# Kernel optimization log

Measured on AMD Instinct MI355X. Metric: run time of the kernel, lower is better.

The kernel has to match this reference:

```python
import jax, jax.numpy as jnp
import numpy as np

B, F, H = 512, 64, 256
INPUT_LEN, TARGET_LEN = 128, 128


def _gru_step(h, xt, Wih, Whh, bih, bhh):
    # PyTorch GRU cell: gates ordered [r, z, n]
    gi = xt @ Wih.T + bih            # [B, 3H]
    gh = h @ Whh.T + bhh             # [B, 3H]
    ir, iz, inn = jnp.split(gi, 3, axis=-1)
    hr, hz, hn = jnp.split(gh, 3, axis=-1)
    r = jax.nn.sigmoid(ir + hr)
    z = jax.nn.sigmoid(iz + hz)
    n = jnp.tanh(inn + r * hn)
    return (1.0 - z) * n + z * h


def setup_inputs() -> dict:
    key = jax.random.key(0)
    ks = jax.random.split(key, 12)
    s_in = 1.0 / np.sqrt(H)
    x = jax.random.normal(ks[0], (B, INPUT_LEN + TARGET_LEN, F), dtype=jnp.float32)
    u = lambda k, shp: jax.random.uniform(k, shp, jnp.float32, -s_in, s_in)
    return {
        "x": x,
        "enc_Wih": u(ks[1], (3 * H, F)), "enc_Whh": u(ks[2], (3 * H, H)),
        "enc_bih": u(ks[3], (3 * H,)), "enc_bhh": u(ks[4], (3 * H,)),
        "dec_Wih": u(ks[5], (3 * H, F)), "dec_Whh": u(ks[6], (3 * H, H)),
        "dec_bih": u(ks[7], (3 * H,)), "dec_bhh": u(ks[8], (3 * H,)),
        "reg_W": u(ks[9], (F, H)), "reg_b": u(ks[10], (F,)),
        "input_len": INPUT_LEN, "target_len": TARGET_LEN,
    }


def reference(x, enc_Wih, enc_Whh, enc_bih, enc_bhh,
              dec_Wih, dec_Whh, dec_bih, dec_bhh,
              reg_W, reg_b, input_len, target_len):
    source_seq = x[:, :input_len, :]                       # [B, Tin, F]
    b = source_seq.shape[0]

    # Encoder GRU over source sequence, h0 = 0
    def enc_step(h, xt):
        h = _gru_step(h, xt, enc_Wih, enc_Whh, enc_bih, enc_bhh)
        return h, None
    h0 = jnp.zeros((b, enc_Whh.shape[1]), dtype=x.dtype)
    h_enc, _ = jax.lax.scan(enc_step, h0, source_seq.transpose(1, 0, 2))

    # Decoder: eval mode -> teacher forcing prob 0, always feed back own output
    dec_in0 = source_seq[:, -1, :]                         # [B, F]
    def dec_step(carry, _):
        h, inp = carry
        h = _gru_step(h, inp, dec_Wih, dec_Whh, dec_bih, dec_bhh)
        out = h @ reg_W.T + reg_b                          # [B, F]
        return (h, out), out
    (_, _), outs = jax.lax.scan(dec_step, (h_enc, dec_in0), None, length=target_len)
    return outs.transpose(1, 0, 2)                         # [B, Tout, F]
```

## Files before the change

### kernel.cpp

```cpp
#include <hip/hip_runtime.h>
#include <math.h>

#define Bsz 512
#define Fsz 64
#define Hsz 256
#define TSTEPS 128
#define G3 768

#define BG 16
#define HB 16
#define NBLK 256
#define NTHR 256
#define CNT_STRIDE 512
#define POLLER 192

#define AP 264
#define XAP 72

#define OFF_AH  0
#define OFF_AL  16896
#define OFF_XH  33792
#define OFF_XL  38400
#define OFF_RED 43008
#define OFF_B   75776
#define SMEM_BYTES (OFF_B + 512)

typedef float f32x4 __attribute__((ext_vector_type(4)));
typedef short s16x8 __attribute__((ext_vector_type(8)));
typedef unsigned short u16x4 __attribute__((ext_vector_type(4)));
typedef unsigned int  u32x4 __attribute__((ext_vector_type(4)));

#define MF(a,b,c) __builtin_amdgcn_mfma_f32_16x16x32_bf16(a,b,c,0,0,0)

static __device__ __forceinline__ unsigned short bf16_rne(float f){
    union { float f; unsigned u; } v; v.f = f;
    return (unsigned short)((v.u + 0x7FFFu + ((v.u >> 16) & 1u)) >> 16);
}
static __device__ __forceinline__ float bf16_to_f(unsigned short h){
    union { unsigned u; float f; } v; v.u = ((unsigned)h) << 16; return v.f;
}
static __device__ __forceinline__ void split8(const float* p, s16x8& hi, s16x8& lo){
    #pragma unroll
    for (int t = 0; t < 8; ++t){
        float f = p[t];
        unsigned short h = bf16_rne(f);
        hi[t] = (short)h;
        lo[t] = (short)bf16_rne(f - bf16_to_f(h));
    }
}
static __device__ __forceinline__ float sigmoidf_(float v){ return 1.0f/(1.0f + expf(-v)); }

__device__ __forceinline__ u32x4 load_sys_b128u(const unsigned* p){
    u32x4 r;
    asm volatile("global_load_dwordx4 %0, %1, off sc0 sc1" : "=v"(r) : "v"(p) : "memory");
    return r;
}
__device__ __forceinline__ void store_sys_b32u(unsigned* p, unsigned v){
    asm volatile("global_store_dword %0, %1, off sc0 sc1" :: "v"(p), "v"(v) : "memory");
}
__device__ __forceinline__ int load_sys_i32(const int* p){
    int r;
    asm volatile("global_load_dword %0, %1, off sc0 sc1\n\ts_waitcnt vmcnt(0)"
                 : "=v"(r) : "v"(p) : "memory");
    return r;
}
__device__ __forceinline__ void waitcnt0(){ asm volatile("s_waitcnt vmcnt(0)" ::: "memory"); }
__device__ __forceinline__ void regbar(u32x4& v){ asm volatile("" : "+v"(v)); }

extern "C" __global__ void gru_setup(const float* __restrict__ x,
                                     const float* __restrict__ dWih,
                                     const float* __restrict__ dbih,
                                     const float* __restrict__ regW,
                                     const float* __restrict__ regb,
                                     float* __restrict__ Mw,
                                     float* __restrict__ cfold,
                                     float* __restrict__ gi0)
{
    int idx = blockIdx.x*blockDim.x + threadIdx.x;
    if (idx < G3*Hsz) {
        int g = idx >> 8, j = idx & 255;
        float a = 0.f;
        #pragma unroll 8
        for (int f = 0; f < Fsz; ++f) a += dWih[g*Fsz + f]*regW[f*Hsz + j];
        Mw[idx] = a;
    } else if (idx < G3*Hsz + G3) {
        int g = idx - G3*Hsz;
        float a = dbih[g];
        #pragma unroll 8
        for (int f = 0; f < Fsz; ++f) a += dWih[g*Fsz + f]*regb[f];
        cfold[g] = a;
    } else {
        int e = idx - (G3*Hsz + G3);
        if (e < Bsz*G3) {
            int b = e / G3, g = e - b*G3;
            const float* xp = x + (size_t)b*(256*64) + 127*64;
            float a = dbih[g];
            #pragma unroll 8
            for (int f = 0; f < Fsz; ++f) a += xp[f]*dWih[g*Fsz + f];
            gi0[e] = a;
        }
    }
}

extern "C" __global__ void __launch_bounds__(NTHR, 1)
gru_persistent(const float* __restrict__ x,
               const float* __restrict__ eWih, const float* __restrict__ eWhh,
               const float* __restrict__ ebih, const float* __restrict__ ebhh,
               const float* __restrict__ dWhh, const float* __restrict__ dbhh,
               const float* __restrict__ Mw,   const float* __restrict__ cfold,
               const float* __restrict__ gi0,  const float* __restrict__ regW,
               const float* __restrict__ regb,
               unsigned* __restrict__ hbuf, int* __restrict__ cnt,
               float* __restrict__ out)
{
    extern __shared__ char lds[];
    unsigned short* s_ah = (unsigned short*)(lds + OFF_AH);
    unsigned short* s_al = (unsigned short*)(lds + OFF_AL);
    unsigned short* s_xh = (unsigned short*)(lds + OFF_XH);
    unsigned short* s_xl = (unsigned short*)(lds + OFF_XL);
    float* s_red  = (float*)(lds + OFF_RED);
    float* s_bias = (float*)(lds + OFF_B);
    float* s_dbh  = s_bias + 64;
    float* s_b3   = s_bias + 112;

    const int tid  = threadIdx.x;
    const int wv   = tid >> 6;
    const int lane = tid & 63;
    const int quad = lane >> 4;
    const int lcol = lane & 15;
    const int bg   = blockIdx.x >> 4;
    const int hb   = blockIdx.x & 15;
    const int hcol = hb*16 + lcol;
    int* mycnt = cnt + bg*CNT_STRIDE;
    const f32x4 z4 = {0.f, 0.f, 0.f, 0.f};

    s16x8 wfh[3][2], wfl[3][2];
    s16x8 ufh[3], ufl[3];
    #pragma unroll
    for (int g = 0; g < 3; ++g)
        #pragma unroll
        for (int q = 0; q < 2; ++q)
            split8(eWhh + (size_t)(g*256 + hcol)*256 + wv*64 + q*32 + quad*8,
                   wfh[g][q], wfl[g][q]);
    if (wv < 2){
        #pragma unroll
        for (int g = 0; g < 3; ++g)
            split8(eWih + (size_t)(g*256 + hcol)*64 + wv*32 + quad*8, ufh[g], ufl[g]);
    }
    if (tid < 16){
        int c = hb*16 + tid;
        s_bias[tid]    = ebih[c]       + ebhh[c];
        s_bias[16+tid] = ebih[256+c]   + ebhh[256+c];
        s_bias[32+tid] = ebih[512+c];
        s_bias[48+tid] = ebhh[512+c];
    }
    __syncthreads();

    int parity = 0;

    for (int s = 0; s < TSTEPS; ++s) {
        f32x4 aR[2], aZ[2], aNi[2], aNh[2];
        if (wv == 0){
            float bR = s_bias[lcol], bZ = s_bias[16+lcol];
            float bNi = s_bias[32+lcol], bNh = s_bias[48+lcol];
            #pragma unroll
            for (int m = 0; m < 2; ++m){
                aR[m] = (f32x4){bR,bR,bR,bR}; aZ[m] = (f32x4){bZ,bZ,bZ,bZ};
                aNi[m] = (f32x4){bNi,bNi,bNi,bNi}; aNh[m] = (f32x4){bNh,bNh,bNh,bNh};
            }
        } else {
            #pragma unroll
            for (int m = 0; m < 2; ++m){ aR[m]=z4; aZ[m]=z4; aNi[m]=z4; aNh[m]=z4; }
        }

        #pragma unroll
        for (int jj = 0; jj < 2; ++jj){
            int flat = (wv*2 + jj)*64 + lane;
            int row = flat >> 4, c4 = flat & 15;
            f32x4 xv = *(const f32x4*)(x + (size_t)(bg*32+row)*(256*64) + (size_t)s*64 + c4*4);
            u16x4 xh, xl;
            #pragma unroll
            for (int t = 0; t < 4; ++t){
                unsigned short h = bf16_rne(xv[t]);
                xh[t] = h; xl[t] = bf16_rne(xv[t] - bf16_to_f(h));
            }
            *(u16x4*)(s_xh + row*XAP + c4*4) = xh;
            *(u16x4*)(s_xl + row*XAP + c4*4) = xl;
        }
        __syncthreads();

        if (wv < 2){
            #pragma unroll
            for (int m = 0; m < 2; ++m){
                const int ko = wv*32 + quad*8;
                s16x8 xah = *(const s16x8*)(s_xh + (m*16+lcol)*XAP + ko);
                s16x8 xal = *(const s16x8*)(s_xl + (m*16+lcol)*XAP + ko);
                aR[m]=MF(xah,ufh[0],aR[m]); aR[m]=MF(xah,ufl[0],aR[m]); aR[m]=MF(xal,ufh[0],aR[m]);
                aZ[m]=MF(xah,ufh[1],aZ[m]); aZ[m]=MF(xah,ufl[1],aZ[m]); aZ[m]=MF(xal,ufh[1],aZ[m]);
                aNi[m]=MF(xah,ufh[2],aNi[m]); aNi[m]=MF(xah,ufl[2],aNi[m]); aNi[m]=MF(xal,ufh[2],aNi[m]);
            }
        }

        if (s > 0 && tid == POLLER){
            while (load_sys_i32(mycnt + s) < HB) __builtin_amdgcn_s_sleep(2);
        }
        __syncthreads();

        const unsigned* hin = hbuf + (size_t)parity*Bsz*Hsz;
        {
            u32x4 t[8];
            #pragma unroll
            for (int jj = 0; jj < 8; ++jj){
                int flat = (wv*8 + jj)*64 + lane;
                int row = flat >> 6, c4 = flat & 63;
                t[jj] = load_sys_b128u(hin + (size_t)(bg*32+row)*256 + c4*4);
            }
            waitcnt0();
            #pragma unroll
            for (int jj = 0; jj < 8; ++jj) regbar(t[jj]);
            #pragma unroll
            for (int jj = 0; jj < 8; ++jj){
                int flat = (wv*8 + jj)*64 + lane;
                int row = flat >> 6, c4 = flat & 63;
                u16x4 hh, ll;
                #pragma unroll
                for (int e = 0; e < 4; ++e){
                    unsigned u = t[jj][e];
                    hh[e] = (unsigned short)(u >> 16);
                    ll[e] = (unsigned short)(u & 0xFFFFu);
                }
                *(u16x4*)(s_ah + row*AP + c4*4) = hh;
                *(u16x4*)(s_al + row*AP + c4*4) = ll;
            }
        }
        __syncthreads();

        #pragma unroll
        for (int m = 0; m < 2; ++m){
            #pragma unroll
            for (int q = 0; q < 2; ++q){
                const int ko = wv*64 + q*32 + quad*8;
                s16x8 ah = *(const s16x8*)(s_ah + (m*16+lcol)*AP + ko);
                s16x8 al = *(const s16x8*)(s_al + (m*16+lcol)*AP + ko);
                aR[m]=MF(ah,wfh[0][q],aR[m]); aR[m]=MF(ah,wfl[0][q],aR[m]); aR[m]=MF(al,wfh[0][q],aR[m]);
                aZ[m]=MF(ah,wfh[1][q],aZ[m]); aZ[m]=MF(ah,wfl[1][q],aZ[m]); aZ[m]=MF(al,wfh[1][q],aZ[m]);
                aNh[m]=MF(ah,wfh[2][q],aNh[m]); aNh[m]=MF(ah,wfl[2][q],aNh[m]); aNh[m]=MF(al,wfh[2][q],aNh[m]);
            }
        }

        #pragma unroll
        for (int m = 0; m < 2; ++m){
            f32x4* rp = (f32x4*)s_red + (wv*8 + m*4)*64 + lane;
            rp[0] = aR[m]; rp[64] = aZ[m]; rp[128] = aNi[m]; rp[192] = aNh[m];
        }
        __syncthreads();

        unsigned* hout = hbuf + (size_t)(parity^1)*Bsz*Hsz;
        if (wv < 2){
            const int m = wv;
            f32x4 R = z4, Z = z4, Ni = z4, Nh = z4;
            #pragma unroll
            for (int w = 0; w < 4; ++w){
                const f32x4* rp = (const f32x4*)s_red + (w*8 + m*4)*64 + lane;
                R += rp[0]; Z += rp[64]; Ni += rp[128]; Nh += rp[192];
            }
            #pragma unroll
            for (int j = 0; j < 4; ++j){
                int rl = m*16 + quad*4 + j;
                float r = sigmoidf_(R[j]);
                float z = sigmoidf_(Z[j]);
                float n = tanhf(Ni[j] + r*Nh[j]);
                float hold = bf16_to_f(s_ah[rl*AP + hcol]) + bf16_to_f(s_al[rl*AP + hcol]);
                float hv = (1.0f - z)*n + z*hold;
                unsigned short p1 = bf16_rne(hv);
                unsigned short p0 = bf16_rne(hv - bf16_to_f(p1));
                store_sys_b32u(hout + (size_t)(bg*32+rl)*256 + hcol,
                               (((unsigned)p1) << 16) | (unsigned)p0);
            }
            waitcnt0();
        }
        __syncthreads();
        if (tid == POLLER)
            __hip_atomic_fetch_add(mycnt + s + 1, 1, __ATOMIC_RELAXED,
                                   __HIP_MEMORY_SCOPE_SYSTEM);
        parity ^= 1;
    }

    s16x8 mfh[3][2], mfl[3][2];
    #pragma unroll
    for (int g = 0; g < 3; ++g)
        #pragma unroll
        for (int q = 0; q < 2; ++q){
            split8(dWhh + (size_t)(g*256 + hcol)*256 + wv*64 + q*32 + quad*8,
                   wfh[g][q], wfl[g][q]);
            split8(Mw   + (size_t)(g*256 + hcol)*256 + wv*64 + q*32 + quad*8,
                   mfh[g][q], mfl[g][q]);
        }
    s16x8 rwh[8], rwl[8];
    if (wv >= 2){
        #pragma unroll
        for (int q8 = 0; q8 < 8; ++q8)
            split8(regW + (size_t)(hb*4 + (lcol & 3))*256 + q8*32 + quad*8,
                   rwh[q8], rwl[q8]);
    }
    if (tid < 16){
        int c = hb*16 + tid;
        s_bias[tid]    = cfold[c]     + dbhh[c];
        s_bias[16+tid] = cfold[256+c] + dbhh[256+c];
        s_bias[32+tid] = cfold[512+c];
        s_dbh[tid]     = dbhh[c];
        s_dbh[16+tid]  = dbhh[256+c];
        s_dbh[32+tid]  = dbhh[512+c];
    }
    if (tid < 4) s_b3[tid] = regb[hb*4 + tid];
    __syncthreads();

    for (int i = 0; i < TSTEPS; ++i) {
        const int sflag = TSTEPS + i;

        f32x4 aR[2], aZ[2], aNi[2], aNh[2];
        if (wv == 0){
            if (i == 0){
                #pragma unroll
                for (int m = 0; m < 2; ++m){
                    #pragma unroll
                    for (int j = 0; j < 4; ++j){
                        int grow_ = bg*32 + m*16 + quad*4 + j;
                        const float* gp = gi0 + (size_t)grow_*G3 + hcol;
                        aR[m][j]  = gp[0]   + s_dbh[lcol];
                        aZ[m][j]  = gp[256] + s_dbh[16+lcol];
                        aNi[m][j] = gp[512];
                        aNh[m][j] = s_dbh[32+lcol];
                    }
                }
            } else {
                float bR = s_bias[lcol], bZ = s_bias[16+lcol];
                float bNi = s_bias[32+lcol], bNh = s_dbh[32+lcol];
                #pragma unroll
                for (int m = 0; m < 2; ++m){
                    aR[m] = (f32x4){bR,bR,bR,bR}; aZ[m] = (f32x4){bZ,bZ,bZ,bZ};
                    aNi[m] = (f32x4){bNi,bNi,bNi,bNi}; aNh[m] = (f32x4){bNh,bNh,bNh,bNh};
                }
            }
        } else {
            #pragma unroll
            for (int m = 0; m < 2; ++m){ aR[m]=z4; aZ[m]=z4; aNi[m]=z4; aNh[m]=z4; }
        }

        if (tid == POLLER){
            while (load_sys_i32(mycnt + sflag) < HB) __builtin_amdgcn_s_sleep(2);
        }
        __syncthreads();

        const unsigned* hin = hbuf + (size_t)parity*Bsz*Hsz;
        {
            u32x4 t[8];
            #pragma unroll
            for (int jj = 0; jj < 8; ++jj){
                int flat = (wv*8 + jj)*64 + lane;
                int row = flat >> 6, c4 = flat & 63;
                t[jj] = load_sys_b128u(hin + (size_t)(bg*32+row)*256 + c4*4);
            }
            waitcnt0();
            #pragma unroll
            for (int jj = 0; jj < 8; ++jj) regbar(t[jj]);
            #pragma unroll
            for (int jj = 0; jj < 8; ++jj){
                int flat = (wv*8 + jj)*64 + lane;
                int row = flat >> 6, c4 = flat & 63;
                u16x4 hh, ll;
                #pragma unroll
                for (int e = 0; e < 4; ++e){
                    unsigned u = t[jj][e];
                    hh[e] = (unsigned short)(u >> 16);
                    ll[e] = (unsigned short)(u & 0xFFFFu);
                }
                *(u16x4*)(s_ah + row*AP + c4*4) = hh;
                *(u16x4*)(s_al + row*AP + c4*4) = ll;
            }
        }
        __syncthreads();

        #pragma unroll
        for (int m = 0; m < 2; ++m){
            #pragma unroll
            for (int q = 0; q < 2; ++q){
                const int ko = wv*64 + q*32 + quad*8;
                s16x8 ah = *(const s16x8*)(s_ah + (m*16+lcol)*AP + ko);
                s16x8 al = *(const s16x8*)(s_al + (m*16+lcol)*AP + ko);
                aR[m]=MF(ah,wfh[0][q],aR[m]); aR[m]=MF(ah,wfl[0][q],aR[m]); aR[m]=MF(al,wfh[0][q],aR[m]);
                aZ[m]=MF(ah,wfh[1][q],aZ[m]); aZ[m]=MF(ah,wfl[1][q],aZ[m]); aZ[m]=MF(al,wfh[1][q],aZ[m]);
                aNh[m]=MF(ah,wfh[2][q],aNh[m]); aNh[m]=MF(ah,wfl[2][q],aNh[m]); aNh[m]=MF(al,wfh[2][q],aNh[m]);
                if (i > 0){
                    aR[m]=MF(ah,mfh[0][q],aR[m]); aR[m]=MF(ah,mfl[0][q],aR[m]); aR[m]=MF(al,mfh[0][q],aR[m]);
                    aZ[m]=MF(ah,mfh[1][q],aZ[m]); aZ[m]=MF(ah,mfl[1][q],aZ[m]); aZ[m]=MF(al,mfh[1][q],aZ[m]);
                    aNi[m]=MF(ah,mfh[2][q],aNi[m]); aNi[m]=MF(ah,mfl[2][q],aNi[m]); aNi[m]=MF(al,mfh[2][q],aNi[m]);
                }
            }
        }

        #pragma unroll
        for (int m = 0; m < 2; ++m){
            f32x4* rp = (f32x4*)s_red + (wv*8 + m*4)*64 + lane;
            rp[0] = aR[m]; rp[64] = aZ[m]; rp[128] = aNi[m]; rp[192] = aNh[m];
        }
        __syncthreads();

        unsigned* hout = hbuf + (size_t)(parity^1)*Bsz*Hsz;
        if (wv < 2){
            const int m = wv;
            f32x4 R = z4, Z = z4, Ni = z4, Nh = z4;
            #pragma unroll
            for (int w = 0; w < 4; ++w){
                const f32x4* rp = (const f32x4*)s_red + (w*8 + m*4)*64 + lane;
                R += rp[0]; Z += rp[64]; Ni += rp[128]; Nh += rp[192];
            }
            #pragma unroll
            for (int j = 0; j < 4; ++j){
                int rl = m*16 + quad*4 + j;
                float r = sigmoidf_(R[j]);
                float z = sigmoidf_(Z[j]);
                float n = tanhf(Ni[j] + r*Nh[j]);
                float hold = bf16_to_f(s_ah[rl*AP + hcol]) + bf16_to_f(s_al[rl*AP + hcol]);
                float hv = (1.0f - z)*n + z*hold;
                unsigned short p1 = bf16_rne(hv);
                unsigned short p0 = bf16_rne(hv - bf16_to_f(p1));
                store_sys_b32u(hout + (size_t)(bg*32+rl)*256 + hcol,
                               (((unsigned)p1) << 16) | (unsigned)p0);
            }
            waitcnt0();
        } else if (i >= 1){
            const int m = wv - 2;
            float b3 = s_b3[lcol & 3];
            f32x4 oa = (f32x4){b3, b3, b3, b3};
            #pragma unroll
            for (int q8 = 0; q8 < 8; ++q8){
                const int ko = q8*32 + quad*8;
                s16x8 ah = *(const s16x8*)(s_ah + (m*16+lcol)*AP + ko);
                s16x8 al = *(const s16x8*)(s_al + (m*16+lcol)*AP + ko);
                oa = MF(ah, rwh[q8], oa); oa = MF(ah, rwl[q8], oa); oa = MF(al, rwh[q8], oa);
            }
            if (lcol < 4){
                #pragma unroll
                for (int j = 0; j < 4; ++j)
                    out[(size_t)(bg*32 + m*16 + quad*4 + j)*(TSTEPS*Fsz)
                        + (size_t)(i-1)*Fsz + hb*4 + lcol] = oa[j];
            }
        }
        __syncthreads();
        if (tid == POLLER)
            __hip_atomic_fetch_add(mycnt + sflag + 1, 1, __ATOMIC_RELAXED,
                                   __HIP_MEMORY_SCOPE_SYSTEM);
        parity ^= 1;
    }

    {
        if (tid == POLLER){
            while (load_sys_i32(mycnt + 2*TSTEPS) < HB) __builtin_amdgcn_s_sleep(2);
        }
        __syncthreads();
        const unsigned* hin = hbuf + (size_t)parity*Bsz*Hsz;
        {
            u32x4 t[8];
            #pragma unroll
            for (int jj = 0; jj < 8; ++jj){
                int flat = (wv*8 + jj)*64 + lane;
                int row = flat >> 6, c4 = flat & 63;
                t[jj] = load_sys_b128u(hin + (size_t)(bg*32+row)*256 + c4*4);
            }
            waitcnt0();
            #pragma unroll
            for (int jj = 0; jj < 8; ++jj) regbar(t[jj]);
            #pragma unroll
            for (int jj = 0; jj < 8; ++jj){
                int flat = (wv*8 + jj)*64 + lane;
                int row = flat >> 6, c4 = flat & 63;
                u16x4 hh, ll;
                #pragma unroll
                for (int e = 0; e < 4; ++e){
                    unsigned u = t[jj][e];
                    hh[e] = (unsigned short)(u >> 16);
                    ll[e] = (unsigned short)(u & 0xFFFFu);
                }
                *(u16x4*)(s_ah + row*AP + c4*4) = hh;
                *(u16x4*)(s_al + row*AP + c4*4) = ll;
            }
        }
        __syncthreads();
        if (wv >= 2){
            const int m = wv - 2;
            float b3 = s_b3[lcol & 3];
            f32x4 oa = (f32x4){b3, b3, b3, b3};
            #pragma unroll
            for (int q8 = 0; q8 < 8; ++q8){
                const int ko = q8*32 + quad*8;
                s16x8 ah = *(const s16x8*)(s_ah + (m*16+lcol)*AP + ko);
                s16x8 al = *(const s16x8*)(s_al + (m*16+lcol)*AP + ko);
                oa = MF(ah, rwh[q8], oa); oa = MF(ah, rwl[q8], oa); oa = MF(al, rwh[q8], oa);
            }
            if (lcol < 4){
                #pragma unroll
                for (int j = 0; j < 4; ++j)
                    out[(size_t)(bg*32 + m*16 + quad*4 + j)*(TSTEPS*Fsz)
                        + (size_t)(TSTEPS-1)*Fsz + hb*4 + lcol] = oa[j];
            }
        }
    }
}

extern "C" void kernel_launch(void* const* d_in, const int* in_sizes, int n_in,
                              void* d_out, int out_size, void* d_ws, size_t ws_size,
                              hipStream_t stream)
{
    (void)in_sizes; (void)n_in; (void)out_size; (void)ws_size;
    const float* x    = (const float*)d_in[0];
    const float* eWih = (const float*)d_in[1];
    const float* eWhh = (const float*)d_in[2];
    const float* ebih = (const float*)d_in[3];
    const float* ebhh = (const float*)d_in[4];
    const float* dWih = (const float*)d_in[5];
    const float* dWhh = (const float*)d_in[6];
    const float* dbih = (const float*)d_in[7];
    const float* dbhh = (const float*)d_in[8];
    const float* regW = (const float*)d_in[9];
    const float* regb = (const float*)d_in[10];
    float* out = (float*)d_out;

    unsigned* hbuf = (unsigned*)d_ws;
    float* Mw    = (float*)d_ws + 2*Bsz*Hsz;
    float* gi0   = Mw + G3*Hsz;
    float* cfold = gi0 + Bsz*G3;
    int*   cnt   = (int*)(cfold + 1024);

    hipMemsetAsync(hbuf, 0, (size_t)Bsz*Hsz*sizeof(unsigned), stream);
    hipMemsetAsync(cnt, 0, (size_t)BG*CNT_STRIDE*sizeof(int), stream);

    hipLaunchKernelGGL(gru_setup, dim3(2307), dim3(256), 0, stream,
                       x, dWih, dbih, regW, regb, Mw, cfold, gi0);

    hipFuncSetAttribute((const void*)gru_persistent,
                        hipFuncAttributeMaxDynamicSharedMemorySize, SMEM_BYTES);

    void* args[] = { (void*)&x, (void*)&eWih, (void*)&eWhh, (void*)&ebih, (void*)&ebhh,
                     (void*)&dWhh, (void*)&dbhh, (void*)&Mw, (void*)&cfold, (void*)&gi0,
                     (void*)&regW, (void*)&regb, (void*)&hbuf, (void*)&cnt, (void*)&out };
    hipError_t rc = hipLaunchCooperativeKernel((const void*)gru_persistent,
                                               dim3(NBLK), dim3(NTHR), args,
                                               SMEM_BYTES, stream);
    if (rc != hipSuccess) {
        hipLaunchKernelGGL(gru_persistent, dim3(NBLK), dim3(NTHR), SMEM_BYTES, stream,
                           x, eWih, eWhh, ebih, ebhh, dWhh, dbhh, Mw, cfold, gi0,
                           regW, regb, hbuf, cnt, out);
    }
}
```

Measured before the change: 1.184 ms.

## Replace counter barrier with per-wave canaries and tagged h values, drop LDS staging

Merges the encoder, decoder and final output loops into one unified step loop. The single polling thread and atomic counter are replaced by per-wave canary flags, which every wave polls with a wave-wide vote, plus 2-bit step tags packed into the low bits of each stored hidden value. Each wave now loads its MFMA operands for the previous hidden state straight from global memory into registers instead of staging them through LDS. The regression output is spread across all waves and reduced through a double-buffered LDS area. This removes several block-wide barriers and LDS round trips per step, at the cost of a tiny precision loss from the tag bits and more redundant global loads.

After: 1.327 ms. 1.12x slower.

```diff
diff --git a/kernel.cpp b/kernel.cpp
--- a/kernel.cpp
+++ b/kernel.cpp
@@ -11,23 +11,13 @@
 #define HB 16
 #define NBLK 256
 #define NTHR 256
-#define CNT_STRIDE 512
-#define POLLER 192
-
-#define AP 264
-#define XAP 72
-
-#define OFF_AH  0
-#define OFF_AL  16896
-#define OFF_XH  33792
-#define OFF_XL  38400
-#define OFF_RED 43008
-#define OFF_B   75776
+
+#define RED_SLOTS 40
+#define OFF_B (2*RED_SLOTS*64*16)
 #define SMEM_BYTES (OFF_B + 512)
 
 typedef float f32x4 __attribute__((ext_vector_type(4)));
 typedef short s16x8 __attribute__((ext_vector_type(8)));
-typedef unsigned short u16x4 __attribute__((ext_vector_type(4)));
 typedef unsigned int  u32x4 __attribute__((ext_vector_type(4)));
 
 #define MF(a,b,c) __builtin_amdgcn_mfma_f32_16x16x32_bf16(a,b,c,0,0,0)
@@ -55,6 +45,11 @@
     asm volatile("global_load_dwordx4 %0, %1, off sc0 sc1" : "=v"(r) : "v"(p) : "memory");
     return r;
 }
+__device__ __forceinline__ unsigned load_sys_b32u_nw(const unsigned* p){
+    unsigned r;
+    asm volatile("global_load_dword %0, %1, off sc0 sc1" : "=v"(r) : "v"(p) : "memory");
+    return r;
+}
 __device__ __forceinline__ void store_sys_b32u(unsigned* p, unsigned v){
     asm volatile("global_store_dword %0, %1, off sc0 sc1" :: "v"(p), "v"(v) : "memory");
 }
@@ -66,6 +61,15 @@
 }
 __device__ __forceinline__ void waitcnt0(){ asm volatile("s_waitcnt vmcnt(0)" ::: "memory"); }
 __device__ __forceinline__ void regbar(u32x4& v){ asm volatile("" : "+v"(v)); }
+__device__ __forceinline__ void regbar32(unsigned& v){ asm volatile("" : "+v"(v)); }
+
+static __device__ __forceinline__ void unpack8(const u32x4 a, const u32x4 b, s16x8& hi, s16x8& lo){
+    #pragma unroll
+    for (int e = 0; e < 4; ++e){
+        hi[e]   = (short)(a[e] >> 16);  lo[e]   = (short)(a[e] & 0xFFFFu);
+        hi[4+e] = (short)(b[e] >> 16);  lo[4+e] = (short)(b[e] & 0xFFFFu);
+    }
+}
 
 extern "C" __global__ void gru_setup(const float* __restrict__ x,
                                      const float* __restrict__ dWih,
@@ -110,15 +114,11 @@
                const float* __restrict__ Mw,   const float* __restrict__ cfold,
                const float* __restrict__ gi0,  const float* __restrict__ regW,
                const float* __restrict__ regb,
-               unsigned* __restrict__ hbuf, int* __restrict__ cnt,
+               unsigned* __restrict__ hbuf, unsigned* __restrict__ canary,
                float* __restrict__ out)
 {
     extern __shared__ char lds[];
-    unsigned short* s_ah = (unsigned short*)(lds + OFF_AH);
-    unsigned short* s_al = (unsigned short*)(lds + OFF_AL);
-    unsigned short* s_xh = (unsigned short*)(lds + OFF_XH);
-    unsigned short* s_xl = (unsigned short*)(lds + OFF_XL);
-    float* s_red  = (float*)(lds + OFF_RED);
+    f32x4* s_redv = (f32x4*)lds;
     float* s_bias = (float*)(lds + OFF_B);
     float* s_dbh  = s_bias + 64;
     float* s_b3   = s_bias + 112;
@@ -131,21 +131,26 @@
     const int bg   = blockIdx.x >> 4;
     const int hb   = blockIdx.x & 15;
     const int hcol = hb*16 + lcol;
-    int* mycnt = cnt + bg*CNT_STRIDE;
+    const int mw   = wv & 1;
+    const int kh   = wv >> 1;
+    const int jb   = kh*2;
+    const int hr0  = mw*16 + quad*4 + jb;
     const f32x4 z4 = {0.f, 0.f, 0.f, 0.f};
+
+    unsigned* mycan = canary + ((size_t)bg*64 + hb*4 + wv)*4;
+    const int* canp = (const int*)canary + ((size_t)bg*64 + lane)*4;
+    const int  can_mine = ((lane >> 2) == hb);
 
     s16x8 wfh[3][2], wfl[3][2];
     s16x8 ufh[3], ufl[3];
+    s16x8 rwh[2], rwl[2];
     #pragma unroll
-    for (int g = 0; g < 3; ++g)
+    for (int g = 0; g < 3; ++g){
         #pragma unroll
         for (int q = 0; q < 2; ++q)
             split8(eWhh + (size_t)(g*256 + hcol)*256 + wv*64 + q*32 + quad*8,
                    wfh[g][q], wfl[g][q]);
-    if (wv < 2){
-        #pragma unroll
-        for (int g = 0; g < 3; ++g)
-            split8(eWih + (size_t)(g*256 + hcol)*64 + wv*32 + quad*8, ufh[g], ufl[g]);
+        split8(eWih + (size_t)(g*256 + hcol)*64 + kh*32 + quad*8, ufh[g], ufl[g]);
     }
     if (tid < 16){
         int c = hb*16 + tid;
@@ -156,173 +161,61 @@
     }
     __syncthreads();
 
-    int parity = 0;
-
-    for (int s = 0; s < TSTEPS; ++s) {
-        f32x4 aR[2], aZ[2], aNi[2], aNh[2];
-        if (wv == 0){
-            float bR = s_bias[lcol], bZ = s_bias[16+lcol];
-            float bNi = s_bias[32+lcol], bNh = s_bias[48+lcol];
-            #pragma unroll
-            for (int m = 0; m < 2; ++m){
-                aR[m] = (f32x4){bR,bR,bR,bR}; aZ[m] = (f32x4){bZ,bZ,bZ,bZ};
-                aNi[m] = (f32x4){bNi,bNi,bNi,bNi}; aNh[m] = (f32x4){bNh,bNh,bNh,bNh};
-            }
-        } else {
-            #pragma unroll
-            for (int m = 0; m < 2; ++m){ aR[m]=z4; aZ[m]=z4; aNi[m]=z4; aNh[m]=z4; }
-        }
-
-        #pragma unroll
-        for (int jj = 0; jj < 2; ++jj){
-            int flat = (wv*2 + jj)*64 + lane;
-            int row = flat >> 4, c4 = flat & 15;
-            f32x4 xv = *(const f32x4*)(x + (size_t)(bg*32+row)*(256*64) + (size_t)s*64 + c4*4);
-            u16x4 xh, xl;
-            #pragma unroll
-            for (int t = 0; t < 4; ++t){
-                unsigned short h = bf16_rne(xv[t]);
-                xh[t] = h; xl[t] = bf16_rne(xv[t] - bf16_to_f(h));
-            }
-            *(u16x4*)(s_xh + row*XAP + c4*4) = xh;
-            *(u16x4*)(s_xl + row*XAP + c4*4) = xl;
-        }
-        __syncthreads();
-
-        if (wv < 2){
-            #pragma unroll
-            for (int m = 0; m < 2; ++m){
-                const int ko = wv*32 + quad*8;
-                s16x8 xah = *(const s16x8*)(s_xh + (m*16+lcol)*XAP + ko);
-                s16x8 xal = *(const s16x8*)(s_xl + (m*16+lcol)*XAP + ko);
-                aR[m]=MF(xah,ufh[0],aR[m]); aR[m]=MF(xah,ufl[0],aR[m]); aR[m]=MF(xal,ufh[0],aR[m]);
-                aZ[m]=MF(xah,ufh[1],aZ[m]); aZ[m]=MF(xah,ufl[1],aZ[m]); aZ[m]=MF(xal,ufh[1],aZ[m]);
-                aNi[m]=MF(xah,ufh[2],aNi[m]); aNi[m]=MF(xah,ufl[2],aNi[m]); aNi[m]=MF(xal,ufh[2],aNi[m]);
-            }
-        }
-
-        if (s > 0 && tid == POLLER){
-            while (load_sys_i32(mycnt + s) < HB) __builtin_amdgcn_s_sleep(2);
-        }
-        __syncthreads();
-
-        const unsigned* hin = hbuf + (size_t)parity*Bsz*Hsz;
-        {
-            u32x4 t[8];
-            #pragma unroll
-            for (int jj = 0; jj < 8; ++jj){
-                int flat = (wv*8 + jj)*64 + lane;
-                int row = flat >> 6, c4 = flat & 63;
-                t[jj] = load_sys_b128u(hin + (size_t)(bg*32+row)*256 + c4*4);
-            }
-            waitcnt0();
-            #pragma unroll
-            for (int jj = 0; jj < 8; ++jj) regbar(t[jj]);
-            #pragma unroll
-            for (int jj = 0; jj < 8; ++jj){
-                int flat = (wv*8 + jj)*64 + lane;
-                int row = flat >> 6, c4 = flat & 63;
-                u16x4 hh, ll;
-                #pragma unroll
-                for (int e = 0; e < 4; ++e){
-                    unsigned u = t[jj][e];
-                    hh[e] = (unsigned short)(u >> 16);
-                    ll[e] = (unsigned short)(u & 0xFFFFu);
+    for (int g = 0; g <= 2*TSTEPS; ++g){
+        const bool enc  = (g < TSTEPS);
+        const bool last = (g == 2*TSTEPS);
+        const int  p    = g & 1;
+        const unsigned tag  = (unsigned)((g >> 1) & 3);
+        const unsigned otag = (unsigned)(((g+1) >> 1) & 3);
+        const unsigned* hin = hbuf + (size_t)(g & 1)*Bsz*Hsz;
+        unsigned* hout = hbuf + (size_t)((g+1) & 1)*Bsz*Hsz;
+
+        if (g == TSTEPS){
+            #pragma unroll
+            for (int gg = 0; gg < 3; ++gg)
+                #pragma unroll
+                for (int q = 0; q < 2; ++q)
+                    split8(dWhh + (size_t)(gg*256 + hcol)*256 + wv*64 + q*32 + quad*8,
+                           wfh[gg][q], wfl[gg][q]);
+            #pragma unroll
+            for (int q = 0; q < 2; ++q){
+                split8(Mw   + (size_t)(2*256 + hcol)*256 + wv*64 + q*32 + quad*8,
+                       ufh[q], ufl[q]);
+                split8(regW + (size_t)(hb*4 + (lcol & 3))*256 + wv*64 + q*32 + quad*8,
+                       rwh[q], rwl[q]);
+            }
+            if (tid < 16){
+                int c = hb*16 + tid;
+                s_bias[tid]    = cfold[c]     + dbhh[c];
+                s_bias[16+tid] = cfold[256+c] + dbhh[256+c];
+                s_bias[32+tid] = cfold[512+c];
+                s_dbh[tid]     = dbhh[c];
+                s_dbh[16+tid]  = dbhh[256+c];
+                s_dbh[32+tid]  = dbhh[512+c];
+            }
+            if (tid < 4) s_b3[tid] = regb[hb*4 + tid];
+            __syncthreads();
+        }
+        if (g == TSTEPS + 1){
+            #pragma unroll
+            for (int gg = 0; gg < 2; ++gg)
+                #pragma unroll
+                for (int q = 0; q < 2; ++q){
+                    float tmp[8];
+                    const float* pa = dWhh + (size_t)(gg*256 + hcol)*256 + wv*64 + q*32 + quad*8;
+                    const float* pb = Mw   + (size_t)(gg*256 + hcol)*256 + wv*64 + q*32 + quad*8;
+                    #pragma unroll
+                    for (int t2 = 0; t2 < 8; ++t2) tmp[t2] = pa[t2] + pb[t2];
+                    split8(tmp, wfh[gg][q], wfl[gg][q]);
                 }
-                *(u16x4*)(s_ah + row*AP + c4*4) = hh;
-                *(u16x4*)(s_al + row*AP + c4*4) = ll;
-            }
-        }
-        __syncthreads();
-
-        #pragma unroll
-        for (int m = 0; m < 2; ++m){
-            #pragma unroll
-            for (int q = 0; q < 2; ++q){
-                const int ko = wv*64 + q*32 + quad*8;
-                s16x8 ah = *(const s16x8*)(s_ah + (m*16+lcol)*AP + ko);
-                s16x8 al = *(const s16x8*)(s_al + (m*16+lcol)*AP + ko);
-                aR[m]=MF(ah,wfh[0][q],aR[m]); aR[m]=MF(ah,wfl[0][q],aR[m]); aR[m]=MF(al,wfh[0][q],aR[m]);
-                aZ[m]=MF(ah,wfh[1][q],aZ[m]); aZ[m]=MF(ah,wfl[1][q],aZ[m]); aZ[m]=MF(al,wfh[1][q],aZ[m]);
-                aNh[m]=MF(ah,wfh[2][q],aNh[m]); aNh[m]=MF(ah,wfl[2][q],aNh[m]); aNh[m]=MF(al,wfh[2][q],aNh[m]);
-            }
-        }
-
-        #pragma unroll
-        for (int m = 0; m < 2; ++m){
-            f32x4* rp = (f32x4*)s_red + (wv*8 + m*4)*64 + lane;
-            rp[0] = aR[m]; rp[64] = aZ[m]; rp[128] = aNi[m]; rp[192] = aNh[m];
-        }
-        __syncthreads();
-
-        unsigned* hout = hbuf + (size_t)(parity^1)*Bsz*Hsz;
-        if (wv < 2){
-            const int m = wv;
-            f32x4 R = z4, Z = z4, Ni = z4, Nh = z4;
-            #pragma unroll
-            for (int w = 0; w < 4; ++w){
-                const f32x4* rp = (const f32x4*)s_red + (w*8 + m*4)*64 + lane;
-                R += rp[0]; Z += rp[64]; Ni += rp[128]; Nh += rp[192];
-            }
-            #pragma unroll
-            for (int j = 0; j < 4; ++j){
-                int rl = m*16 + quad*4 + j;
-                float r = sigmoidf_(R[j]);
-                float z = sigmoidf_(Z[j]);
-                float n = tanhf(Ni[j] + r*Nh[j]);
-                float hold = bf16_to_f(s_ah[rl*AP + hcol]) + bf16_to_f(s_al[rl*AP + hcol]);
-                float hv = (1.0f - z)*n + z*hold;
-                unsigned short p1 = bf16_rne(hv);
-                unsigned short p0 = bf16_rne(hv - bf16_to_f(p1));
-                store_sys_b32u(hout + (size_t)(bg*32+rl)*256 + hcol,
-                               (((unsigned)p1) << 16) | (unsigned)p0);
-            }
-            waitcnt0();
-        }
-        __syncthreads();
-        if (tid == POLLER)
-            __hip_atomic_fetch_add(mycnt + s + 1, 1, __ATOMIC_RELAXED,
-                                   __HIP_MEMORY_SCOPE_SYSTEM);
-        parity ^= 1;
-    }
-
-    s16x8 mfh[3][2], mfl[3][2];
-    #pragma unroll
-    for (int g = 0; g < 3; ++g)
-        #pragma unroll
-        for (int q = 0; q < 2; ++q){
-            split8(dWhh + (size_t)(g*256 + hcol)*256 + wv*64 + q*32 + quad*8,
-                   wfh[g][q], wfl[g][q]);
-            split8(Mw   + (size_t)(g*256 + hcol)*256 + wv*64 + q*32 + quad*8,
-                   mfh[g][q], mfl[g][q]);
-        }
-    s16x8 rwh[8], rwl[8];
-    if (wv >= 2){
-        #pragma unroll
-        for (int q8 = 0; q8 < 8; ++q8)
-            split8(regW + (size_t)(hb*4 + (lcol & 3))*256 + q8*32 + quad*8,
-                   rwh[q8], rwl[q8]);
-    }
-    if (tid < 16){
-        int c = hb*16 + tid;
-        s_bias[tid]    = cfold[c]     + dbhh[c];
-        s_bias[16+tid] = cfold[256+c] + dbhh[256+c];
-        s_bias[32+tid] = cfold[512+c];
-        s_dbh[tid]     = dbhh[c];
-        s_dbh[16+tid]  = dbhh[256+c];
-        s_dbh[32+tid]  = dbhh[512+c];
-    }
-    if (tid < 4) s_b3[tid] = regb[hb*4 + tid];
-    __syncthreads();
-
-    for (int i = 0; i < TSTEPS; ++i) {
-        const int sflag = TSTEPS + i;
-
-        f32x4 aR[2], aZ[2], aNi[2], aNh[2];
-        if (wv == 0){
-            if (i == 0){
-                #pragma unroll
-                for (int m = 0; m < 2; ++m){
+        }
+
+        f32x4 aR[2], aZ[2], aNi[2], aNh[2], oa[2];
+        oa[0] = z4; oa[1] = z4;
+        if (wv == 0 && !last){
+            if (g == TSTEPS){
+                #pragma unroll
+                for (int m = 0; m < 2; ++m)
                     #pragma unroll
                     for (int j = 0; j < 4; ++j){
                         int grow_ = bg*32 + m*16 + quad*4 + j;
@@ -332,10 +225,9 @@
                         aNi[m][j] = gp[512];
                         aNh[m][j] = s_dbh[32+lcol];
                     }
-                }
             } else {
-                float bR = s_bias[lcol], bZ = s_bias[16+lcol];
-                float bNi = s_bias[32+lcol], bNh = s_dbh[32+lcol];
+                float bR = s_bias[lcol], bZ = s_bias[16+lcol], bNi = s_bias[32+lcol];
+                float bNh = enc ? s_bias[48+lcol] : s_dbh[32+lcol];
                 #pragma unroll
                 for (int m = 0; m < 2; ++m){
                     aR[m] = (f32x4){bR,bR,bR,bR}; aZ[m] = (f32x4){bZ,bZ,bZ,bZ};
@@ -347,162 +239,150 @@
             for (int m = 0; m < 2; ++m){ aR[m]=z4; aZ[m]=z4; aNi[m]=z4; aNh[m]=z4; }
         }
 
-        if (tid == POLLER){
-            while (load_sys_i32(mycnt + sflag) < HB) __builtin_amdgcn_s_sleep(2);
-        }
-        __syncthreads();
-
-        const unsigned* hin = hbuf + (size_t)parity*Bsz*Hsz;
+        f32x4 xv0, xv1;
+        if (enc){
+            const float* xp = x + (size_t)(bg*32 + mw*16 + lcol)*(256*64)
+                                + (size_t)g*64 + kh*32 + quad*8;
+            xv0 = *(const f32x4*)xp;
+            xv1 = *(const f32x4*)(xp + 4);
+        }
+
+        if (g){
+            while (1){
+                int v = load_sys_i32(canp);
+                if (__all(can_mine | (v >= g))) break;
+                __builtin_amdgcn_s_sleep(1);
+            }
+        }
+
+        const unsigned* ab = hin + (size_t)(bg*32 + lcol)*256 + wv*64 + quad*8;
+        u32x4 t[8];
+        #pragma unroll
+        for (int m = 0; m < 2; ++m)
+            #pragma unroll
+            for (int q = 0; q < 2; ++q)
+                #pragma unroll
+                for (int h4 = 0; h4 < 2; ++h4)
+                    t[m*4+q*2+h4] = load_sys_b128u(ab + m*4096 + q*32 + h4*4);
+        const unsigned* hoA = hin + (size_t)(bg*32 + hr0)*256 + hcol;
+        unsigned ho0 = load_sys_b32u_nw(hoA);
+        unsigned ho1 = load_sys_b32u_nw(hoA + 256);
+
+        if (enc){
+            float xf[8];
+            #pragma unroll
+            for (int e = 0; e < 4; ++e){ xf[e] = xv0[e]; xf[4+e] = xv1[e]; }
+            s16x8 xh, xl;
+            split8(xf, xh, xl);
+            #define XMF(M) { \
+                aR[M] =MF(xh,ufh[0],aR[M]);  aR[M] =MF(xh,ufl[0],aR[M]);  aR[M] =MF(xl,ufh[0],aR[M]);  \
+                aZ[M] =MF(xh,ufh[1],aZ[M]);  aZ[M] =MF(xh,ufl[1],aZ[M]);  aZ[M] =MF(xl,ufh[1],aZ[M]);  \
+                aNi[M]=MF(xh,ufh[2],aNi[M]); aNi[M]=MF(xh,ufl[2],aNi[M]); aNi[M]=MF(xl,ufh[2],aNi[M]); }
+            if (mw == 0) XMF(0) else XMF(1)
+            #undef XMF
+        }
+
         {
-            u32x4 t[8];
-            #pragma unroll
-            for (int jj = 0; jj < 8; ++jj){
-                int flat = (wv*8 + jj)*64 + lane;
-                int row = flat >> 6, c4 = flat & 63;
-                t[jj] = load_sys_b128u(hin + (size_t)(bg*32+row)*256 + c4*4);
-            }
-            waitcnt0();
-            #pragma unroll
-            for (int jj = 0; jj < 8; ++jj) regbar(t[jj]);
-            #pragma unroll
-            for (int jj = 0; jj < 8; ++jj){
-                int flat = (wv*8 + jj)*64 + lane;
-                int row = flat >> 6, c4 = flat & 63;
-                u16x4 hh, ll;
-                #pragma unroll
-                for (int e = 0; e < 4; ++e){
-                    unsigned u = t[jj][e];
-                    hh[e] = (unsigned short)(u >> 16);
-                    ll[e] = (unsigned short)(u & 0xFFFFu);
-                }
-                *(u16x4*)(s_ah + row*AP + c4*4) = hh;
-                *(u16x4*)(s_al + row*AP + c4*4) = ll;
-            }
-        }
-        __syncthreads();
+            unsigned done = 0;
+            while (1){
+                waitcnt0();
+                #pragma unroll
+                for (int jj = 0; jj < 8; ++jj) regbar(t[jj]);
+                regbar32(ho0); regbar32(ho1);
+                unsigned nd = done;
+                #pragma unroll
+                for (int jj = 0; jj < 8; ++jj)
+                    if (!((nd >> jj) & 1u))
+                        if (((t[jj][0]&3u)==tag) && ((t[jj][1]&3u)==tag) &&
+                            ((t[jj][2]&3u)==tag) && ((t[jj][3]&3u)==tag)) nd |= (1u << jj);
+                if (!((nd >> 8) & 1u) && ((ho0 & 3u) == tag)) nd |= 0x100u;
+                if (!((nd >> 9) & 1u) && ((ho1 & 3u) == tag)) nd |= 0x200u;
+                done = nd;
+                if (__all((int)(done == 0x3FFu))) break;
+                __builtin_amdgcn_s_sleep(1);
+                #pragma unroll
+                for (int m = 0; m < 2; ++m)
+                    #pragma unroll
+                    for (int q = 0; q < 2; ++q)
+                        #pragma unroll
+                        for (int h4 = 0; h4 < 2; ++h4){
+                            const int jj = m*4+q*2+h4;
+                            if (!((done >> jj) & 1u))
+                                t[jj] = load_sys_b128u(ab + m*4096 + q*32 + h4*4);
+                        }
+                if (!((done >> 8) & 1u)) ho0 = load_sys_b32u_nw(hoA);
+                if (!((done >> 9) & 1u)) ho1 = load_sys_b32u_nw(hoA + 256);
+            }
+        }
 
         #pragma unroll
         for (int m = 0; m < 2; ++m){
             #pragma unroll
             for (int q = 0; q < 2; ++q){
-                const int ko = wv*64 + q*32 + quad*8;
-                s16x8 ah = *(const s16x8*)(s_ah + (m*16+lcol)*AP + ko);
-                s16x8 al = *(const s16x8*)(s_al + (m*16+lcol)*AP + ko);
-                aR[m]=MF(ah,wfh[0][q],aR[m]); aR[m]=MF(ah,wfl[0][q],aR[m]); aR[m]=MF(al,wfh[0][q],aR[m]);
-                aZ[m]=MF(ah,wfh[1][q],aZ[m]); aZ[m]=MF(ah,wfl[1][q],aZ[m]); aZ[m]=MF(al,wfh[1][q],aZ[m]);
-                aNh[m]=MF(ah,wfh[2][q],aNh[m]); aNh[m]=MF(ah,wfl[2][q],aNh[m]); aNh[m]=MF(al,wfh[2][q],aNh[m]);
-                if (i > 0){
-                    aR[m]=MF(ah,mfh[0][q],aR[m]); aR[m]=MF(ah,mfl[0][q],aR[m]); aR[m]=MF(al,mfh[0][q],aR[m]);
-                    aZ[m]=MF(ah,mfh[1][q],aZ[m]); aZ[m]=MF(ah,mfl[1][q],aZ[m]); aZ[m]=MF(al,mfh[1][q],aZ[m]);
-                    aNi[m]=MF(ah,mfh[2][q],aNi[m]); aNi[m]=MF(ah,mfl[2][q],aNi[m]); aNi[m]=MF(al,mfh[2][q],aNi[m]);
+                s16x8 ah, al;
+                unpack8(t[m*4+q*2], t[m*4+q*2+1], ah, al);
+                if (!last){
+                    aR[m]=MF(ah,wfh[0][q],aR[m]); aR[m]=MF(ah,wfl[0][q],aR[m]); aR[m]=MF(al,wfh[0][q],aR[m]);
+                    aZ[m]=MF(ah,wfh[1][q],aZ[m]); aZ[m]=MF(ah,wfl[1][q],aZ[m]); aZ[m]=MF(al,wfh[1][q],aZ[m]);
+                    aNh[m]=MF(ah,wfh[2][q],aNh[m]); aNh[m]=MF(ah,wfl[2][q],aNh[m]); aNh[m]=MF(al,wfh[2][q],aNh[m]);
+                    if (!enc && g > TSTEPS){
+                        aNi[m]=MF(ah,ufh[q],aNi[m]); aNi[m]=MF(ah,ufl[q],aNi[m]); aNi[m]=MF(al,ufh[q],aNi[m]);
+                    }
                 }
-            }
-        }
-
-        #pragma unroll
-        for (int m = 0; m < 2; ++m){
-            f32x4* rp = (f32x4*)s_red + (wv*8 + m*4)*64 + lane;
-            rp[0] = aR[m]; rp[64] = aZ[m]; rp[128] = aNi[m]; rp[192] = aNh[m];
+                if (g >= TSTEPS + 1){
+                    oa[m]=MF(ah,rwh[q],oa[m]); oa[m]=MF(ah,rwl[q],oa[m]); oa[m]=MF(al,rwh[q],oa[m]);
+                }
+            }
+        }
+
+        if (!last){
+            f32x4* rp = s_redv + ((size_t)p*RED_SLOTS + wv*8)*64 + lane;
+            rp[0]   = aR[0]; rp[64]  = aZ[0]; rp[128] = aNi[0]; rp[192] = aNh[0];
+            rp[256] = aR[1]; rp[320] = aZ[1]; rp[384] = aNi[1]; rp[448] = aNh[1];
+        }
+        if (g >= TSTEPS + 1){
+            f32x4* op = s_redv + ((size_t)p*RED_SLOTS + 32 + wv*2)*64 + lane;
+            op[0] = oa[0]; op[64] = oa[1];
         }
         __syncthreads();
 
-        unsigned* hout = hbuf + (size_t)(parity^1)*Bsz*Hsz;
-        if (wv < 2){
-            const int m = wv;
+        if (!last){
             f32x4 R = z4, Z = z4, Ni = z4, Nh = z4;
             #pragma unroll
-            for (int w = 0; w < 4; ++w){
-                const f32x4* rp = (const f32x4*)s_red + (w*8 + m*4)*64 + lane;
+            for (int w2 = 0; w2 < 4; ++w2){
+                const f32x4* rp = s_redv + ((size_t)p*RED_SLOTS + w2*8 + mw*4)*64 + lane;
                 R += rp[0]; Z += rp[64]; Ni += rp[128]; Nh += rp[192];
             }
-            #pragma unroll
-            for (int j = 0; j < 4; ++j){
-                int rl = m*16 + quad*4 + j;
-                float r = sigmoidf_(R[j]);
-                float z = sigmoidf_(Z[j]);
-                float n = tanhf(Ni[j] + r*Nh[j]);
-                float hold = bf16_to_f(s_ah[rl*AP + hcol]) + bf16_to_f(s_al[rl*AP + hcol]);
-                float hv = (1.0f - z)*n + z*hold;
-                unsigned short p1 = bf16_rne(hv);
-                unsigned short p0 = bf16_rne(hv - bf16_to_f(p1));
-                store_sys_b32u(hout + (size_t)(bg*32+rl)*256 + hcol,
-                               (((unsigned)p1) << 16) | (unsigned)p0);
-            }
-            waitcnt0();
-        } else if (i >= 1){
-            const int m = wv - 2;
+            #define EW(J, HW, RO) { \
+                float r = sigmoidf_(R[J]); \
+                float z = sigmoidf_(Z[J]); \
+                float n = tanhf(Ni[J] + r*Nh[J]); \
+                float hold = bf16_to_f((unsigned short)((HW) >> 16)) \
+                           + bf16_to_f((unsigned short)((HW) & 0xFFFFu)); \
+                float hv = (1.0f - z)*n + z*hold; \
+                unsigned short p1 = bf16_rne(hv); \
+                unsigned short p0 = bf16_rne(hv - bf16_to_f(p1)); \
+                store_sys_b32u(hout + (size_t)(bg*32 + hr0 + RO)*256 + hcol, \
+                               (((unsigned)p1) << 16) | ((unsigned)(p0 & 0xFFFCu)) | otag); }
+            if (jb == 0){ EW(0, ho0, 0); EW(1, ho1, 1); }
+            else        { EW(2, ho0, 0); EW(3, ho1, 1); }
+            #undef EW
+            if (lane == 0) store_sys_b32u(mycan, (unsigned)(g + 1));
+        }
+
+        if (g >= TSTEPS + 1 && wv >= 2){
+            const int m2 = wv - 2;
             float b3 = s_b3[lcol & 3];
-            f32x4 oa = (f32x4){b3, b3, b3, b3};
-            #pragma unroll
-            for (int q8 = 0; q8 < 8; ++q8){
-                const int ko = q8*32 + quad*8;
-                s16x8 ah = *(const s16x8*)(s_ah + (m*16+lcol)*AP + ko);
-                s16x8 al = *(const s16x8*)(s_al + (m*16+lcol)*AP + ko);
-                oa = MF(ah, rwh[q8], oa); oa = MF(ah, rwl[q8], oa); oa = MF(al, rwh[q8], oa);
-            }
+            f32x4 ot = {b3, b3, b3, b3};
+            #pragma unroll
+            for (int w2 = 0; w2 < 4; ++w2)
+                ot += s_redv[((size_t)p*RED_SLOTS + 32 + w2*2 + m2)*64 + lane];
             if (lcol < 4){
+                const int oidx = g - TSTEPS - 1;
                 #pragma unroll
                 for (int j = 0; j < 4; ++j)
-                    out[(size_t)(bg*32 + m*16 + quad*4 + j)*(TSTEPS*Fsz)
-                        + (size_t)(i-1)*Fsz + hb*4 + lcol] = oa[j];
-            }
-        }
-        __syncthreads();
-        if (tid == POLLER)
-            __hip_atomic_fetch_add(mycnt + sflag + 1, 1, __ATOMIC_RELAXED,
-                                   __HIP_MEMORY_SCOPE_SYSTEM);
-        parity ^= 1;
-    }
-
-    {
-        if (tid == POLLER){
-            while (load_sys_i32(mycnt + 2*TSTEPS) < HB) __builtin_amdgcn_s_sleep(2);
-        }
-        __syncthreads();
-        const unsigned* hin = hbuf + (size_t)parity*Bsz*Hsz;
-        {
-            u32x4 t[8];
-            #pragma unroll
-            for (int jj = 0; jj < 8; ++jj){
-                int flat = (wv*8 + jj)*64 + lane;
-                int row = flat >> 6, c4 = flat & 63;
-                t[jj] = load_sys_b128u(hin + (size_t)(bg*32+row)*256 + c4*4);
-            }
-            waitcnt0();
-            #pragma unroll
-            for (int jj = 0; jj < 8; ++jj) regbar(t[jj]);
-            #pragma unroll
-            for (int jj = 0; jj < 8; ++jj){
-                int flat = (wv*8 + jj)*64 + lane;
-                int row = flat >> 6, c4 = flat & 63;
-                u16x4 hh, ll;
-                #pragma unroll
-                for (int e = 0; e < 4; ++e){
-                    unsigned u = t[jj][e];
-                    hh[e] = (unsigned short)(u >> 16);
-                    ll[e] = (unsigned short)(u & 0xFFFFu);
-                }
-                *(u16x4*)(s_ah + row*AP + c4*4) = hh;
-                *(u16x4*)(s_al + row*AP + c4*4) = ll;
-            }
-        }
-        __syncthreads();
-        if (wv >= 2){
-            const int m = wv - 2;
-            float b3 = s_b3[lcol & 3];
-            f32x4 oa = (f32x4){b3, b3, b3, b3};
-            #pragma unroll
-            for (int q8 = 0; q8 < 8; ++q8){
-                const int ko = q8*32 + quad*8;
-                s16x8 ah = *(const s16x8*)(s_ah + (m*16+lcol)*AP + ko);
-                s16x8 al = *(const s16x8*)(s_al + (m*16+lcol)*AP + ko);
-                oa = MF(ah, rwh[q8], oa); oa = MF(ah, rwl[q8], oa); oa = MF(al, rwh[q8], oa);
-            }
-            if (lcol < 4){
-                #pragma unroll
-                for (int j = 0; j < 4; ++j)
-                    out[(size_t)(bg*32 + m*16 + quad*4 + j)*(TSTEPS*Fsz)
-                        + (size_t)(TSTEPS-1)*Fsz + hb*4 + lcol] = oa[j];
+                    out[(size_t)(bg*32 + m2*16 + quad*4 + j)*(TSTEPS*Fsz)
+                        + (size_t)oidx*Fsz + hb*4 + lcol] = ot[j];
             }
         }
     }
@@ -530,10 +410,11 @@
     float* Mw    = (float*)d_ws + 2*Bsz*Hsz;
     float* gi0   = Mw + G3*Hsz;
     float* cfold = gi0 + Bsz*G3;
-    int*   cnt   = (int*)(cfold + 1024);
+    unsigned* canary = (unsigned*)(cfold + 1024);
 
     hipMemsetAsync(hbuf, 0, (size_t)Bsz*Hsz*sizeof(unsigned), stream);
-    hipMemsetAsync(cnt, 0, (size_t)BG*CNT_STRIDE*sizeof(int), stream);
+    hipMemsetAsync(hbuf + (size_t)Bsz*Hsz, 3, (size_t)Bsz*Hsz*sizeof(unsigned), stream);
+    hipMemsetAsync(canary, 0, (size_t)BG*64*4*sizeof(unsigned), stream);
 
     hipLaunchKernelGGL(gru_setup, dim3(2307), dim3(256), 0, stream,
                        x, dWih, dbih, regW, regb, Mw, cfold, gi0);
@@ -543,13 +424,13 @@
 
     void* args[] = { (void*)&x, (void*)&eWih, (void*)&eWhh, (void*)&ebih, (void*)&ebhh,
                      (void*)&dWhh, (void*)&dbhh, (void*)&Mw, (void*)&cfold, (void*)&gi0,
-                     (void*)&regW, (void*)&regb, (void*)&hbuf, (void*)&cnt, (void*)&out };
+                     (void*)&regW, (void*)&regb, (void*)&hbuf, (void*)&canary, (void*)&out };
     hipError_t rc = hipLaunchCooperativeKernel((const void*)gru_persistent,
                                                dim3(NBLK), dim3(NTHR), args,
                                                SMEM_BYTES, stream);
     if (rc != hipSuccess) {
         hipLaunchKernelGGL(gru_persistent, dim3(NBLK), dim3(NTHR), SMEM_BYTES, stream,
                            x, eWih, eWhh, ebih, ebhh, dWhh, dbhh, Mw, cfold, gi0,
-                           regW, regb, hbuf, cnt, out);
-    }
-}
+                           regW, regb, hbuf, canary, out);
+    }
+}
```
